# Kernel tuning notes

Measured on AMD Instinct MI355X. Metric: run time of the kernel, lower is better.

The kernel has to match this reference:

```python
import jax, jax.numpy as jnp
import numpy as np

N = 8192


def setup_inputs() -> dict:
    key = jax.random.key(0)
    k1, k2 = jax.random.split(key)
    pred = jax.random.normal(k1, (N, 1), dtype=jnp.float32)
    ytime = jax.random.uniform(k2, (N, 1), dtype=jnp.float32)
    return {"pred": pred, "ytime": ytime}


def reference(pred, ytime):
    # Cox partial-likelihood loss, censoring = -1 => all samples are events.
    # Original math (after sorting by ytime ascending):
    #   sorted_exp[j] = sum_{i >= j} exp(sp[i] - sp[j])
    #   loss = mean_j log(sorted_exp[j])
    # which equals revcumlogsumexp(sp)[j] - sp[j]; same math, O(N) and stable.
    idx = jnp.argsort(ytime[:, 0])           # [N] sort order by event time
    sp = pred[idx, 0]                        # [N] risk scores in time order
    censor = jnp.ones_like(sp)               # censoring < 0 branch: all ones
    # log sum_{i >= j} exp(sp[i]) computed as reversed cumulative logsumexp
    log_risk_set = jax.lax.cumlogsumexp(sp[::-1])[::-1]   # [N]
    neg_log_exp = jnp.sum((log_risk_set - sp) * censor)
    return neg_log_exp / jnp.sum(censor)
```

## Files before the change

### kernel.cpp

```cpp
#include <hip/hip_runtime.h>
#include <math.h>


#define COX_N 8192
#define BLOCK 256
#define JPB 64
#define CI 1024
#define GJ (COX_N / JPB)
#define GI (COX_N / CI)
#define JPT 4
#define JGRP (JPB / JPT)
#define ISL (BLOCK / JGRP)
#define IPT (CI / ISL)

typedef __attribute__((ext_vector_type(2))) unsigned long long ull2;

__global__ __launch_bounds__(BLOCK) void cox_main(const float* __restrict__ pred,
                                                  const float* __restrict__ ytime,
                                                  float* __restrict__ partial) {
    __shared__ unsigned long long key_s[CI];
    __shared__ float e_s[CI];
    __shared__ float red[JPB][ISL + 1];

    const int tid = threadIdx.x;
    const int bj = blockIdx.x;
    const int bi = blockIdx.y;
    const int ibase = bi * CI;

    {
        const float4* y4 = (const float4*)(ytime + ibase);
        const float4* p4 = (const float4*)(pred + ibase);
        float4 y = y4[tid];
        float4 p = p4[tid];
        int gi = ibase + tid * 4;
        key_s[tid * 4 + 0] = ((unsigned long long)__float_as_uint(y.x) << 13) | (unsigned)(gi + 0);
        key_s[tid * 4 + 1] = ((unsigned long long)__float_as_uint(y.y) << 13) | (unsigned)(gi + 1);
        key_s[tid * 4 + 2] = ((unsigned long long)__float_as_uint(y.z) << 13) | (unsigned)(gi + 2);
        key_s[tid * 4 + 3] = ((unsigned long long)__float_as_uint(y.w) << 13) | (unsigned)(gi + 3);
        e_s[tid * 4 + 0] = __expf(p.x);
        e_s[tid * 4 + 1] = __expf(p.y);
        e_s[tid * 4 + 2] = __expf(p.z);
        e_s[tid * 4 + 3] = __expf(p.w);
    }

    const int jg = tid & (JGRP - 1);
    const int is = tid >> 4;
    const int j0 = bj * JPB + jg * JPT;

    unsigned long long jkey[JPT];
    float r[JPT];
#pragma unroll
    for (int q = 0; q < JPT; ++q) {
        int j = j0 + q;
        jkey[q] = ((unsigned long long)__float_as_uint(ytime[j]) << 13) | (unsigned)j;
        r[q] = 0.0f;
    }

    __syncthreads();

    const ull2* k2 = (const ull2*)(key_s + is * IPT);
    const float2* e2 = (const float2*)(e_s + is * IPT);
#pragma unroll 8
    for (int t = 0; t < IPT / 2; ++t) {
        ull2 k = k2[t];
        float2 e = e2[t];
#pragma unroll
        for (int q = 0; q < JPT; ++q) {
            r[q] += (k.x >= jkey[q]) ? e.x : 0.0f;
            r[q] += (k.y >= jkey[q]) ? e.y : 0.0f;
        }
    }

#pragma unroll
    for (int q = 0; q < JPT; ++q) red[jg * JPT + q][is] = r[q];
    __syncthreads();

    if (tid < JPB) {
        float s = 0.0f;
#pragma unroll
        for (int t = 0; t < ISL; ++t) s += red[tid][t];
        partial[bi * COX_N + bj * JPB + tid] = s;
    }
}

__global__ __launch_bounds__(256) void cox_fin(const float* __restrict__ partial,
                                               const float* __restrict__ pred,
                                               float* __restrict__ bsum) {
    const int tid = threadIdx.x;
    const int j = blockIdx.x * 256 + tid;
    float rsum = 0.0f;
#pragma unroll
    for (int c = 0; c < GI; ++c) rsum += partial[c * COX_N + j];
    float loss = logf(rsum) - pred[j];
#pragma unroll
    for (int off = 32; off > 0; off >>= 1) loss += __shfl_down(loss, off);
    __shared__ float wsum[4];
    if ((tid & 63) == 0) wsum[tid >> 6] = loss;
    __syncthreads();
    if (tid == 0) bsum[blockIdx.x] = wsum[0] + wsum[1] + wsum[2] + wsum[3];
}

__global__ void cox_fin2(const float* __restrict__ bsum, float* __restrict__ out) {
    const int tid = threadIdx.x;
    float v = (tid < 32) ? bsum[tid] : 0.0f;
#pragma unroll
    for (int off = 32; off > 0; off >>= 1) v += __shfl_down(v, off);
    if (tid == 0) out[0] = v * (1.0f / (float)COX_N);
}

extern "C" void kernel_launch(void* const* d_in, const int* in_sizes, int n_in,
                              void* d_out, int out_size, void* d_ws, size_t ws_size,
                              hipStream_t stream) {
    const float* pred  = (const float*)d_in[0];
    const float* ytime = (const float*)d_in[1];
    float* partial = (float*)d_ws;
    float* bsum    = (float*)d_ws + GI * COX_N;
    float* out     = (float*)d_out;

    cox_main<<<dim3(GJ, GI), BLOCK, 0, stream>>>(pred, ytime, partial);
    cox_fin<<<COX_N / 256, 256, 0, stream>>>(partial, pred, bsum);
    cox_fin2<<<1, 64, 0, stream>>>(bsum, out);
}
```

Measured before the change: 15.59 us.

## Widen per-thread j tile, pad shared rows, merge final reductions into one kernel

The main kernel now gives each thread 8 j values instead of 4, which halves the number of i-slices per thread group and doubles the comparisons done per shared-memory load. The key and exp arrays are stored with padded per-slice strides to spread LDS bank accesses. The two finishing kernels are merged into a single 1024-thread block that reads partial sums with float4 loads and reduces directly to the output, which removes one kernel launch. The trade-offs are higher register pressure in the main kernel and a final pass that runs on a single CU.

```diff
diff --git a/kernel.cpp b/kernel.cpp
--- a/kernel.cpp
+++ b/kernel.cpp
@@ -5,21 +5,23 @@
 #define COX_N 8192
 #define BLOCK 256
 #define JPB 64
+#define JPT 8
+#define JGRP (JPB / JPT)
+#define ISL (BLOCK / JGRP)
 #define CI 1024
+#define IPT (CI / ISL)
 #define GJ (COX_N / JPB)
 #define GI (COX_N / CI)
-#define JPT 4
-#define JGRP (JPB / JPT)
-#define ISL (BLOCK / JGRP)
-#define IPT (CI / ISL)
+#define KSTR (IPT + 2)
+#define ESTR (IPT + 2)
 
 typedef __attribute__((ext_vector_type(2))) unsigned long long ull2;
 
 __global__ __launch_bounds__(BLOCK) void cox_main(const float* __restrict__ pred,
                                                   const float* __restrict__ ytime,
                                                   float* __restrict__ partial) {
-    __shared__ unsigned long long key_s[CI];
-    __shared__ float e_s[CI];
+    __shared__ unsigned long long key_s[ISL * KSTR];
+    __shared__ float e_s[ISL * ESTR];
     __shared__ float red[JPB][ISL + 1];
 
     const int tid = threadIdx.x;
@@ -32,19 +34,24 @@
         const float4* p4 = (const float4*)(pred + ibase);
         float4 y = y4[tid];
         float4 p = p4[tid];
-        int gi = ibase + tid * 4;
-        key_s[tid * 4 + 0] = ((unsigned long long)__float_as_uint(y.x) << 13) | (unsigned)(gi + 0);
-        key_s[tid * 4 + 1] = ((unsigned long long)__float_as_uint(y.y) << 13) | (unsigned)(gi + 1);
-        key_s[tid * 4 + 2] = ((unsigned long long)__float_as_uint(y.z) << 13) | (unsigned)(gi + 2);
-        key_s[tid * 4 + 3] = ((unsigned long long)__float_as_uint(y.w) << 13) | (unsigned)(gi + 3);
-        e_s[tid * 4 + 0] = __expf(p.x);
-        e_s[tid * 4 + 1] = __expf(p.y);
-        e_s[tid * 4 + 2] = __expf(p.z);
-        e_s[tid * 4 + 3] = __expf(p.w);
+        int li = tid * 4;
+        int s  = li / IPT;
+        int pth = li % IPT;
+        unsigned long long* kd = key_s + s * KSTR + pth;
+        float* ed = e_s + s * ESTR + pth;
+        int gi = ibase + li;
+        kd[0] = ((unsigned long long)__float_as_uint(y.x) << 13) | (unsigned)(gi + 0);
+        kd[1] = ((unsigned long long)__float_as_uint(y.y) << 13) | (unsigned)(gi + 1);
+        kd[2] = ((unsigned long long)__float_as_uint(y.z) << 13) | (unsigned)(gi + 2);
+        kd[3] = ((unsigned long long)__float_as_uint(y.w) << 13) | (unsigned)(gi + 3);
+        ed[0] = __expf(p.x);
+        ed[1] = __expf(p.y);
+        ed[2] = __expf(p.z);
+        ed[3] = __expf(p.w);
     }
 
     const int jg = tid & (JGRP - 1);
-    const int is = tid >> 4;
+    const int is = tid >> 3;
     const int j0 = bj * JPB + jg * JPT;
 
     unsigned long long jkey[JPT];
@@ -58,8 +65,8 @@
 
     __syncthreads();
 
-    const ull2* k2 = (const ull2*)(key_s + is * IPT);
-    const float2* e2 = (const float2*)(e_s + is * IPT);
+    const ull2* k2 = (const ull2*)(key_s + is * KSTR);
+    const float2* e2 = (const float2*)(e_s + is * ESTR);
 #pragma unroll 8
     for (int t = 0; t < IPT / 2; ++t) {
         ull2 k = k2[t];
@@ -83,29 +90,49 @@
     }
 }
 
-__global__ __launch_bounds__(256) void cox_fin(const float* __restrict__ partial,
-                                               const float* __restrict__ pred,
-                                               float* __restrict__ bsum) {
+__global__ __launch_bounds__(1024) void cox_fin(const float* __restrict__ partial,
+                                                const float* __restrict__ pred,
+                                                float* __restrict__ out) {
     const int tid = threadIdx.x;
-    const int j = blockIdx.x * 256 + tid;
-    float rsum = 0.0f;
+    const int j0 = tid * 8;
+
+    float rsum[8];
 #pragma unroll
-    for (int c = 0; c < GI; ++c) rsum += partial[c * COX_N + j];
-    float loss = logf(rsum) - pred[j];
+    for (int q = 0; q < 8; ++q) rsum[q] = 0.0f;
+    const float4* pa4 = (const float4*)partial;
+#pragma unroll
+    for (int c = 0; c < GI; ++c) {
+        float4 a = pa4[(c * COX_N + j0) / 4];
+        float4 b = pa4[(c * COX_N + j0) / 4 + 1];
+        rsum[0] += a.x; rsum[1] += a.y; rsum[2] += a.z; rsum[3] += a.w;
+        rsum[4] += b.x; rsum[5] += b.y; rsum[6] += b.z; rsum[7] += b.w;
+    }
+    const float4* pr4 = (const float4*)pred;
+    float4 pa = pr4[j0 / 4];
+    float4 pb = pr4[j0 / 4 + 1];
+
+    float loss = 0.0f;
+    loss += logf(rsum[0]) - pa.x;
+    loss += logf(rsum[1]) - pa.y;
+    loss += logf(rsum[2]) - pa.z;
+    loss += logf(rsum[3]) - pa.w;
+    loss += logf(rsum[4]) - pb.x;
+    loss += logf(rsum[5]) - pb.y;
+    loss += logf(rsum[6]) - pb.z;
+    loss += logf(rsum[7]) - pb.w;
+
 #pragma unroll
     for (int off = 32; off > 0; off >>= 1) loss += __shfl_down(loss, off);
-    __shared__ float wsum[4];
+
+    __shared__ float wsum[16];
     if ((tid & 63) == 0) wsum[tid >> 6] = loss;
     __syncthreads();
-    if (tid == 0) bsum[blockIdx.x] = wsum[0] + wsum[1] + wsum[2] + wsum[3];
-}
-
-__global__ void cox_fin2(const float* __restrict__ bsum, float* __restrict__ out) {
-    const int tid = threadIdx.x;
-    float v = (tid < 32) ? bsum[tid] : 0.0f;
+    if (tid < 64) {
+        float v = (tid < 16) ? wsum[tid] : 0.0f;
 #pragma unroll
-    for (int off = 32; off > 0; off >>= 1) v += __shfl_down(v, off);
-    if (tid == 0) out[0] = v * (1.0f / (float)COX_N);
+        for (int off = 8; off > 0; off >>= 1) v += __shfl_down(v, off);
+        if (tid == 0) out[0] = v * (1.0f / (float)COX_N);
+    }
 }
 
 extern "C" void kernel_launch(void* const* d_in, const int* in_sizes, int n_in,
@@ -114,10 +141,8 @@
     const float* pred  = (const float*)d_in[0];
     const float* ytime = (const float*)d_in[1];
     float* partial = (float*)d_ws;
-    float* bsum    = (float*)d_ws + GI * COX_N;
     float* out     = (float*)d_out;
 
     cox_main<<<dim3(GJ, GI), BLOCK, 0, stream>>>(pred, ytime, partial);
-    cox_fin<<<COX_N / 256, 256, 0, stream>>>(partial, pred, bsum);
-    cox_fin2<<<1, 64, 0, stream>>>(bsum, out);
+    cox_fin<<<1, 1024, 0, stream>>>(partial, pred, out);
 }
```

New measurement: 16.54 us. 6.1% more time.

## Fuse partial reduction into main kernel with full-range blocks and float compares

Applied to the files above, without the earlier changes.

Each block now stages all samples' (ytime, exp(pred)) pairs in padded shared memory and computes complete risk-set sums for 16 rows. It then applies log and subtracts pred in-kernel and emits one partial per block. This removes the partial-sum buffer and one kernel launch. Comparisons use 32-bit floats instead of 64-bit keys with an index tie-break, so tied times are all included. The exp work per block grows and shared memory use rises sharply, which may lower occupancy.

```diff
diff --git a/kernel.cpp b/kernel.cpp
--- a/kernel.cpp
+++ b/kernel.cpp
@@ -4,108 +4,102 @@
 
 #define COX_N 8192
 #define BLOCK 256
-#define JPB 64
-#define CI 1024
+#define JPB 16
+#define JPT 8
+#define JGRP 2
+#define ISL 128
+#define IPS (COX_N / ISL)
 #define GJ (COX_N / JPB)
-#define GI (COX_N / CI)
-#define JPT 4
-#define JGRP (JPB / JPT)
-#define ISL (BLOCK / JGRP)
-#define IPT (CI / ISL)
-
-typedef __attribute__((ext_vector_type(2))) unsigned long long ull2;
+#define STR (2 * IPS + 6)
 
 __global__ __launch_bounds__(BLOCK) void cox_main(const float* __restrict__ pred,
                                                   const float* __restrict__ ytime,
-                                                  float* __restrict__ partial) {
-    __shared__ unsigned long long key_s[CI];
-    __shared__ float e_s[CI];
-    __shared__ float red[JPB][ISL + 1];
+                                                  float* __restrict__ bsum) {
+    __shared__ float ye_s[ISL * STR];
+    __shared__ float red[4][JGRP][JPT];
 
     const int tid = threadIdx.x;
     const int bj = blockIdx.x;
-    const int bi = blockIdx.y;
-    const int ibase = bi * CI;
 
-    {
-        const float4* y4 = (const float4*)(ytime + ibase);
-        const float4* p4 = (const float4*)(pred + ibase);
-        float4 y = y4[tid];
-        float4 p = p4[tid];
-        int gi = ibase + tid * 4;
-        key_s[tid * 4 + 0] = ((unsigned long long)__float_as_uint(y.x) << 13) | (unsigned)(gi + 0);
-        key_s[tid * 4 + 1] = ((unsigned long long)__float_as_uint(y.y) << 13) | (unsigned)(gi + 1);
-        key_s[tid * 4 + 2] = ((unsigned long long)__float_as_uint(y.z) << 13) | (unsigned)(gi + 2);
-        key_s[tid * 4 + 3] = ((unsigned long long)__float_as_uint(y.w) << 13) | (unsigned)(gi + 3);
-        e_s[tid * 4 + 0] = __expf(p.x);
-        e_s[tid * 4 + 1] = __expf(p.y);
-        e_s[tid * 4 + 2] = __expf(p.z);
-        e_s[tid * 4 + 3] = __expf(p.w);
+    const float4* y4 = (const float4*)ytime;
+    const float4* p4 = (const float4*)pred;
+#pragma unroll
+    for (int w = 0; w < COX_N / 4 / BLOCK; ++w) {
+        int v = tid + w * BLOCK;
+        float4 y = y4[v];
+        float4 p = p4[v];
+        int i = v * 4;
+        int s = i >> 6, pos = i & 63;
+        float2* d2 = (float2*)(ye_s + s * STR + 2 * pos);
+        d2[0] = float2{y.x, __expf(p.x)};
+        d2[1] = float2{y.y, __expf(p.y)};
+        d2[2] = float2{y.z, __expf(p.z)};
+        d2[3] = float2{y.w, __expf(p.w)};
     }
 
     const int jg = tid & (JGRP - 1);
-    const int is = tid >> 4;
+    const int is = tid >> 1;
     const int j0 = bj * JPB + jg * JPT;
 
-    unsigned long long jkey[JPT];
+    float ytj[JPT];
     float r[JPT];
 #pragma unroll
     for (int q = 0; q < JPT; ++q) {
-        int j = j0 + q;
-        jkey[q] = ((unsigned long long)__float_as_uint(ytime[j]) << 13) | (unsigned)j;
+        ytj[q] = ytime[j0 + q];
         r[q] = 0.0f;
     }
 
     __syncthreads();
 
-    const ull2* k2 = (const ull2*)(key_s + is * IPT);
-    const float2* e2 = (const float2*)(e_s + is * IPT);
-#pragma unroll 8
-    for (int t = 0; t < IPT / 2; ++t) {
-        ull2 k = k2[t];
-        float2 e = e2[t];
+    const float2* ye2 = (const float2*)(ye_s + is * STR);
+#pragma unroll 4
+    for (int t = 0; t < IPS; t += 2) {
+        float2 a = ye2[t];
+        float2 b = ye2[t + 1];
 #pragma unroll
         for (int q = 0; q < JPT; ++q) {
-            r[q] += (k.x >= jkey[q]) ? e.x : 0.0f;
-            r[q] += (k.y >= jkey[q]) ? e.y : 0.0f;
+            r[q] += (a.x >= ytj[q]) ? a.y : 0.0f;
+            r[q] += (b.x >= ytj[q]) ? b.y : 0.0f;
         }
     }
 
 #pragma unroll
-    for (int q = 0; q < JPT; ++q) red[jg * JPT + q][is] = r[q];
+    for (int m = 2; m <= 32; m <<= 1) {
+#pragma unroll
+        for (int q = 0; q < JPT; ++q) r[q] += __shfl_xor(r[q], m);
+    }
+    if ((tid & 62) == 0) {
+#pragma unroll
+        for (int q = 0; q < JPT; ++q) red[tid >> 6][tid & 1][q] = r[q];
+    }
     __syncthreads();
 
     if (tid < JPB) {
-        float s = 0.0f;
+        int qg = tid >> 3, q = tid & 7;
+        float S = red[0][qg][q] + red[1][qg][q] + red[2][qg][q] + red[3][qg][q];
+        int j = bj * JPB + qg * JPT + q;
+        float loss = logf(S) - pred[j];
 #pragma unroll
-        for (int t = 0; t < ISL; ++t) s += red[tid][t];
-        partial[bi * COX_N + bj * JPB + tid] = s;
+        for (int off = 8; off > 0; off >>= 1) loss += __shfl_down(loss, off);
+        if (tid == 0) bsum[bj] = loss;
     }
 }
 
-__global__ __launch_bounds__(256) void cox_fin(const float* __restrict__ partial,
-                                               const float* __restrict__ pred,
-                                               float* __restrict__ bsum) {
+__global__ __launch_bounds__(512) void cox_fin(const float* __restrict__ bsum,
+                                               float* __restrict__ out) {
     const int tid = threadIdx.x;
-    const int j = blockIdx.x * 256 + tid;
-    float rsum = 0.0f;
-#pragma unroll
-    for (int c = 0; c < GI; ++c) rsum += partial[c * COX_N + j];
-    float loss = logf(rsum) - pred[j];
-#pragma unroll
-    for (int off = 32; off > 0; off >>= 1) loss += __shfl_down(loss, off);
-    __shared__ float wsum[4];
-    if ((tid & 63) == 0) wsum[tid >> 6] = loss;
-    __syncthreads();
-    if (tid == 0) bsum[blockIdx.x] = wsum[0] + wsum[1] + wsum[2] + wsum[3];
-}
-
-__global__ void cox_fin2(const float* __restrict__ bsum, float* __restrict__ out) {
-    const int tid = threadIdx.x;
-    float v = (tid < 32) ? bsum[tid] : 0.0f;
+    float v = bsum[tid];
 #pragma unroll
     for (int off = 32; off > 0; off >>= 1) v += __shfl_down(v, off);
-    if (tid == 0) out[0] = v * (1.0f / (float)COX_N);
+    __shared__ float w[8];
+    if ((tid & 63) == 0) w[tid >> 6] = v;
+    __syncthreads();
+    if (tid == 0) {
+        float s = 0.0f;
+#pragma unroll
+        for (int k = 0; k < 8; ++k) s += w[k];
+        out[0] = s * (1.0f / (float)COX_N);
+    }
 }
 
 extern "C" void kernel_launch(void* const* d_in, const int* in_sizes, int n_in,
@@ -113,11 +107,9 @@
                               hipStream_t stream) {
     const float* pred  = (const float*)d_in[0];
     const float* ytime = (const float*)d_in[1];
-    float* partial = (float*)d_ws;
-    float* bsum    = (float*)d_ws + GI * COX_N;
-    float* out     = (float*)d_out;
+    float* bsum = (float*)d_ws;
+    float* out  = (float*)d_out;
 
-    cox_main<<<dim3(GJ, GI), BLOCK, 0, stream>>>(pred, ytime, partial);
-    cox_fin<<<COX_N / 256, 256, 0, stream>>>(partial, pred, bsum);
-    cox_fin2<<<1, 64, 0, stream>>>(bsum, out);
+    cox_main<<<GJ, BLOCK, 0, stream>>>(pred, ytime, bsum);
+    cox_fin<<<1, 512, 0, stream>>>(bsum, out);
 }
```

New measurement: 16.12 us. 1.03x slower.
